# Kernel tuning notes

Hardware: AMD Instinct MI355X
Metric: run time of the kernel (lower is better)

The kernel has to match this reference:

```python
import jax, jax.numpy as jnp
import numpy as np

BS, NE, F = 128, 512, 6
HEADS, DPH = 4, 4
N_EMBD = HEADS * DPH  # 16


def setup_inputs() -> dict:
    key = jax.random.key(0)
    k_inp, k_mask, kq, kk, kv, kp = jax.random.split(key, 6)
    inp = jax.random.normal(k_inp, (BS, NE, F), dtype=jnp.float32)
    # binary float mask; guarantee at least one unmasked entity per batch row
    mask = (jax.random.uniform(k_mask, (BS, NE)) < 0.8).astype(jnp.float32)
    mask = mask.at[:, 0].set(1.0)
    std = 1.0 / np.sqrt(N_EMBD)
    Wq = jax.random.normal(kq, (N_EMBD, F), dtype=jnp.float32) * std
    Wk = jax.random.normal(kk, (N_EMBD, F), dtype=jnp.float32) * std
    Wv = jax.random.normal(kv, (N_EMBD, F), dtype=jnp.float32) * std
    Wpost = jax.random.normal(kp, (F, N_EMBD), dtype=jnp.float32) * std
    return {"inp": inp, "mask": mask, "Wq": Wq, "Wk": Wk, "Wv": Wv, "Wpost": Wpost}


def reference(inp, mask, Wq, Wk, Wv, Wpost):
    bs, ne, f = inp.shape
    x_in = inp * mask[:, :, None]                       # mask input entities
    # projections (Linear with weight [out,in]): x @ W.T
    q = (x_in @ Wq.T).reshape(bs, ne, HEADS, DPH)
    k = (x_in @ Wk.T).reshape(bs, ne, HEADS, DPH)
    v = (x_in @ Wv.T).reshape(bs, ne, HEADS, DPH)
    scale = 1.0 / np.sqrt(N_EMBD / HEADS)               # 1/sqrt(4)
    logits = jnp.einsum('bqhd,bkhd->bhqk', q, k) * scale  # [bs,H,NE,NE]
    logits = logits + 1e9 * (mask[:, None, None, :] - 1.0)  # mask keys pre-softmax
    p = jax.nn.softmax(logits, axis=-1)
    p = p * mask[:, None, :, None]                      # zero masked query rows
    att = jnp.einsum('bhqk,bkhd->bqhd', p, v).reshape(bs, ne, N_EMBD)
    x = x_in + att @ Wpost.T                            # residual
    # mask-corrected mean/std normalization over dims [1,2]
    N = jnp.sum(mask, axis=1)[:, None, None]            # [bs,1,1] valid entity count
    mu = jnp.mean(x, axis=(1, 2), keepdims=True) * (ne / N)
    x2 = x + (1.0 - mask[:, :, None]) * mu              # fill masked slots with mu
    m2 = jnp.mean(x2, axis=(1, 2), keepdims=True)
    var = jnp.sum((x2 - m2) ** 2, axis=(1, 2), keepdims=True) / (ne * f - 1)  # unbiased
    std = jnp.sqrt(var) * jnp.sqrt((f * ne - 1.0) / (f * N - 1.0))
    xn = (x - mu) / (std + 1e-6)
    # masked mean pool over entities
    summed = jnp.sum(xn * mask[:, :, None], axis=1)     # [bs,F]
    denom = jnp.sum(mask, axis=1)[:, None]
    return summed / denom
```

## Files before the change

kernel.cpp:

```cpp
#include <hip/hip_runtime.h>
#include <math.h>

#define BS    128
#define NE    512
#define F     6
#define NH    4
#define DPH   4
#define NEMBD 16

#if __has_builtin(__builtin_amdgcn_exp2f)
#define EXP2(x) __builtin_amdgcn_exp2f(x)
#else
#define EXP2(x) exp2f(x)
#endif

typedef float v2f __attribute__((ext_vector_type(2)));

#define CH    8
#define CKEYS 64
#define CPAD  65

__global__ __launch_bounds__(256) void attn_kernel(
    const float* __restrict__ inp, const float* __restrict__ mask,
    const float* __restrict__ Wq, const float* __restrict__ Wk,
    const float* __restrict__ Wv, float* __restrict__ att_out)
{
    const int blk  = blockIdx.x;
    const int b    = blk >> 3;
    const int h    = (blk >> 1) & 3;
    const int half = blk & 1;
    const int t    = threadIdx.x;
    const int c    = t & 7;
    const int g    = t >> 3;

    __shared__ float4 sk[CH * CPAD];
    __shared__ float4 sv[CH * CPAD];
    __shared__ float  sn[4];

    float mw = 0.f;
    #pragma unroll
    for (int s = 0; s < 2; ++s) {
        const int e = t + s * 256;
        const float me = mask[b * NE + e];
        mw += me;
        const float2* rp = (const float2*)(inp + ((size_t)(b * NE + e)) * F);
        const float2 r0 = rp[0], r1 = rp[1], r2 = rp[2];
        const float x0 = r0.x * me, x1 = r0.y * me, x2 = r1.x * me,
                    x3 = r1.y * me, x4 = r2.x * me, x5 = r2.y * me;
        const float* wk = Wk + h * DPH * F;
        const float* wv = Wv + h * DPH * F;
        float kk[DPH], vv[DPH];
        #pragma unroll
        for (int d = 0; d < DPH; ++d) {
            const float* w = wk + d * F;
            kk[d] = x0*w[0] + x1*w[1] + x2*w[2] + x3*w[3] + x4*w[4] + x5*w[5];
            w = wv + d * F;
            vv[d] = x0*w[0] + x1*w[1] + x2*w[2] + x3*w[3] + x4*w[4] + x5*w[5];
        }
        sk[(e >> 6) * CPAD + (e & 63)] = make_float4(kk[0], kk[1], kk[2], kk[3]);
        sv[(e >> 6) * CPAD + (e & 63)] = make_float4(vv[0], vv[1], vv[2], vv[3]);
    }
    #pragma unroll
    for (int off = 32; off >= 1; off >>= 1) mw += __shfl_down(mw, off);
    if ((t & 63) == 0) sn[t >> 6] = mw;

    const float QS = 0.5f * 1.44269504088896340736f;
    v2f qv[4][DPH];
    {
        const float* wq = Wq + h * DPH * F;
        #pragma unroll
        for (int r = 0; r < 8; ++r) {
            const int row = half * 256 + 8 * g + r;
            const float mr = mask[b * NE + row];
            const float2* rp = (const float2*)(inp + ((size_t)(b * NE + row)) * F);
            const float2 r0 = rp[0], r1 = rp[1], r2 = rp[2];
            const float x0 = r0.x * mr, x1 = r0.y * mr, x2 = r1.x * mr,
                        x3 = r1.y * mr, x4 = r2.x * mr, x5 = r2.y * mr;
            #pragma unroll
            for (int d = 0; d < DPH; ++d) {
                const float* w = wq + d * F;
                const float qd = QS * (x0*w[0] + x1*w[1] + x2*w[2] + x3*w[3] + x4*w[4] + x5*w[5]);
                if (r & 1) qv[r >> 1][d].y = qd; else qv[r >> 1][d].x = qd;
            }
        }
    }

    __syncthreads();

    const float Nb = sn[0] + sn[1] + sn[2] + sn[3];
    const float lcorr = 512.0f - Nb;

    const float4* kb = sk + c * CPAD;
    const float4* vb = sv + c * CPAD;
    v2f l2[4], a2[4][DPH];
    #pragma unroll
    for (int p = 0; p < 4; ++p) {
        l2[p] = (v2f)(0.f);
        #pragma unroll
        for (int d = 0; d < DPH; ++d) a2[p][d] = (v2f)(0.f);
    }

    #pragma unroll 4
    for (int j = 0; j < CKEYS; ++j) {
        const float4 kv = kb[j];
        const float4 uv = vb[j];
        const v2f kx = (v2f){kv.x, kv.x}, ky = (v2f){kv.y, kv.y},
                  kz = (v2f){kv.z, kv.z}, kw = (v2f){kv.w, kv.w};
        const v2f ux = (v2f){uv.x, uv.x}, uy = (v2f){uv.y, uv.y},
                  uz = (v2f){uv.z, uv.z}, uw = (v2f){uv.w, uv.w};
        #pragma unroll
        for (int p = 0; p < 4; ++p) {
            v2f s = qv[p][3] * kw;
            s = __builtin_elementwise_fma(qv[p][2], kz, s);
            s = __builtin_elementwise_fma(qv[p][1], ky, s);
            s = __builtin_elementwise_fma(qv[p][0], kx, s);
            v2f e;
            e.x = EXP2(s.x);
            e.y = EXP2(s.y);
            l2[p] += e;
            a2[p][0] = __builtin_elementwise_fma(e, ux, a2[p][0]);
            a2[p][1] = __builtin_elementwise_fma(e, uy, a2[p][1]);
            a2[p][2] = __builtin_elementwise_fma(e, uz, a2[p][2]);
            a2[p][3] = __builtin_elementwise_fma(e, uw, a2[p][3]);
        }
    }

    #pragma unroll
    for (int m = 1; m <= 4; m <<= 1) {
        #pragma unroll
        for (int p = 0; p < 4; ++p) {
            l2[p].x += __shfl_xor(l2[p].x, m);
            l2[p].y += __shfl_xor(l2[p].y, m);
            #pragma unroll
            for (int d = 0; d < DPH; ++d) {
                a2[p][d].x += __shfl_xor(a2[p][d].x, m);
                a2[p][d].y += __shfl_xor(a2[p][d].y, m);
            }
        }
    }

    float lsel = l2[0].x, p0 = a2[0][0].x, p1 = a2[0][1].x,
          p2 = a2[0][2].x, p3 = a2[0][3].x;
    #pragma unroll
    for (int r = 1; r < 8; ++r) {
        if (r == c) {
            const int pp = r >> 1;
            if (r & 1) {
                lsel = l2[pp].y; p0 = a2[pp][0].y; p1 = a2[pp][1].y;
                p2 = a2[pp][2].y; p3 = a2[pp][3].y;
            } else {
                lsel = l2[pp].x; p0 = a2[pp][0].x; p1 = a2[pp][1].x;
                p2 = a2[pp][2].x; p3 = a2[pp][3].x;
            }
        }
    }

    const int row = half * 256 + 8 * g + c;
    const float mi = mask[b * NE + row];
    const float rs = mi / (lsel - lcorr);
    float4* o = (float4*)(att_out + ((size_t)(b * NE + row)) * NEMBD + h * DPH);
    *o = make_float4(p0 * rs, p1 * rs, p2 * rs, p3 * rs);
}

__global__ __launch_bounds__(NE) void epi_kernel(
    const float* __restrict__ inp, const float* __restrict__ mask,
    const float* __restrict__ Wpost, const float* __restrict__ att,
    float* __restrict__ out)
{
    const int b = blockIdx.x;
    const int i = threadIdx.x;
    const int wave = i >> 6;
    const int lane = i & 63;

    __shared__ float swp[F * NEMBD];
    __shared__ float red[64];

    if (i < F * NEMBD) swp[i] = Wpost[i];
    __syncthreads();

    const float mi = mask[b * NE + i];
    const float* row = inp + ((size_t)(b * NE + i)) * F;
    const float* ar  = att + ((size_t)(b * NE + i)) * NEMBD;

    float a[NEMBD];
    #pragma unroll
    for (int t = 0; t < NEMBD; t += 4) {
        const float4 v = *(const float4*)(ar + t);
        a[t] = v.x; a[t+1] = v.y; a[t+2] = v.z; a[t+3] = v.w;
    }

    float x[F];
    #pragma unroll
    for (int f = 0; f < F; ++f) {
        float acc = row[f] * mi;
        #pragma unroll
        for (int t = 0; t < NEMBD; ++t) acc = fmaf(a[t], swp[f * NEMBD + t], acc);
        x[f] = acc;
    }

    float rsum = x[0] + x[1] + x[2] + x[3] + x[4] + x[5];
    float rn = mi;
    #pragma unroll
    for (int off = 32; off >= 1; off >>= 1) {
        rsum += __shfl_down(rsum, off);
        rn   += __shfl_down(rn, off);
    }
    if (lane == 0) { red[wave * 2] = rsum; red[wave * 2 + 1] = rn; }
    __syncthreads();
    float S = 0.f, N = 0.f;
    #pragma unroll
    for (int w = 0; w < 8; ++w) { S += red[w * 2]; N += red[w * 2 + 1]; }

    const float mu     = S / (6.0f * N);
    const float sum_x2 = S + (NE - N) * 6.0f * mu;
    const float m2     = sum_x2 / (NE * 6.0f);
    const float add    = (1.0f - mi) * mu;

    float ss = 0.f;
    #pragma unroll
    for (int f = 0; f < F; ++f) { const float d = x[f] + add - m2; ss = fmaf(d, d, ss); }

    __syncthreads();
    #pragma unroll
    for (int off = 32; off >= 1; off >>= 1) ss += __shfl_down(ss, off);
    if (lane == 0) red[wave] = ss;
    __syncthreads();
    float vs = 0.f;
    #pragma unroll
    for (int w = 0; w < 8; ++w) vs += red[w];

    const float var  = vs / (NE * 6.0f - 1.0f);
    const float stdv = sqrtf(var) * sqrtf((6.0f * NE - 1.0f) / (6.0f * N - 1.0f));
    const float inv  = 1.0f / (stdv + 1e-6f);

    float y[F];
    #pragma unroll
    for (int f = 0; f < F; ++f) y[f] = mi * (x[f] - mu) * inv;

    __syncthreads();
    #pragma unroll
    for (int off = 32; off >= 1; off >>= 1) {
        #pragma unroll
        for (int f = 0; f < F; ++f) y[f] += __shfl_down(y[f], off);
    }
    if (lane == 0) {
        #pragma unroll
        for (int f = 0; f < F; ++f) red[wave * F + f] = y[f];
    }
    __syncthreads();
    if (i < F) {
        float tt = 0.f;
        #pragma unroll
        for (int w = 0; w < 8; ++w) tt += red[w * F + i];
        out[b * F + i] = tt / N;
    }
}

extern "C" void kernel_launch(void* const* d_in, const int* in_sizes, int n_in,
                              void* d_out, int out_size, void* d_ws, size_t ws_size,
                              hipStream_t stream) {
    const float* inp   = (const float*)d_in[0];
    const float* mask  = (const float*)d_in[1];
    const float* Wq    = (const float*)d_in[2];
    const float* Wk    = (const float*)d_in[3];
    const float* Wv    = (const float*)d_in[4];
    const float* Wpost = (const float*)d_in[5];
    float* out = (float*)d_out;
    float* att = (float*)d_ws;

    attn_kernel<<<BS * NH * 2, 256, 0, stream>>>(inp, mask, Wq, Wk, Wv, att);
    epi_kernel <<<BS, NE, 0, stream>>>(inp, mask, Wpost, att, out);
}
```

Baseline: 103.8 us.

## Compact unmasked entities so attention only iterates over active keys and queries

The attention kernel now uses a ballot and an atomic prefix to compact the unmasked entities into contiguous shared-memory slots. Q, K and V are computed only for active entities, and each thread loops over L = ceil(Nk/8) keys instead of all 64, with a correction for zero-padded slots. Waves whose query slots are all beyond Nk exit early. Blocks are merged from 2x256 to one 512-thread block per (batch, head) so each block sees every entity. Masked rows are no longer written, so the epilogue multiplies the attention input by the mask to ignore stale workspace values. In exchange this adds an atomic, extra barriers and shared-memory zeroing, and reduces the number of blocks.

```diff
diff --git a/kernel.cpp b/kernel.cpp
--- a/kernel.cpp
+++ b/kernel.cpp
@@ -8,6 +8,9 @@
 #define DPH   4
 #define NEMBD 16
 
+#define CH    8
+#define CPAD  65
+
 #if __has_builtin(__builtin_amdgcn_exp2f)
 #define EXP2(x) __builtin_amdgcn_exp2f(x)
 #else
@@ -16,79 +19,91 @@
 
 typedef float v2f __attribute__((ext_vector_type(2)));
 
-#define CH    8
-#define CKEYS 64
-#define CPAD  65
-
-__global__ __launch_bounds__(256) void attn_kernel(
+__global__ __launch_bounds__(512) void attn_kernel(
     const float* __restrict__ inp, const float* __restrict__ mask,
     const float* __restrict__ Wq, const float* __restrict__ Wk,
     const float* __restrict__ Wv, float* __restrict__ att_out)
 {
-    const int blk  = blockIdx.x;
-    const int b    = blk >> 3;
-    const int h    = (blk >> 1) & 3;
-    const int half = blk & 1;
+    const int b    = blockIdx.x >> 2;
+    const int h    = blockIdx.x & 3;
     const int t    = threadIdx.x;
     const int c    = t & 7;
     const int g    = t >> 3;
+    const int w    = t >> 6;
+    const int lane = t & 63;
 
     __shared__ float4 sk[CH * CPAD];
     __shared__ float4 sv[CH * CPAD];
-    __shared__ float  sn[4];
-
-    float mw = 0.f;
-    #pragma unroll
-    for (int s = 0; s < 2; ++s) {
-        const int e = t + s * 256;
-        const float me = mask[b * NE + e];
-        mw += me;
-        const float2* rp = (const float2*)(inp + ((size_t)(b * NE + e)) * F);
+    __shared__ float4 sq[576];
+    __shared__ unsigned short rlist[512];
+    __shared__ int scnt;
+    __shared__ int swb[8];
+
+    const float4 z4 = make_float4(0.f, 0.f, 0.f, 0.f);
+    sk[c * CPAD + g] = z4;
+    sv[c * CPAD + g] = z4;
+    sq[9 * g + c]    = z4;
+    if (t == 0) scnt = 0;
+
+    const float me = mask[b * NE + t];
+    const bool act = me > 0.f;
+
+    __syncthreads();
+
+    const unsigned long long ball = __ballot(act);
+    const unsigned int blo = (unsigned int)ball;
+    const unsigned int bhi = (unsigned int)(ball >> 32);
+    const int prefix = __builtin_amdgcn_mbcnt_hi(bhi,
+                        __builtin_amdgcn_mbcnt_lo(blo, 0));
+    if (lane == 0) swb[w] = atomicAdd(&scnt, (int)__popcll(ball));
+
+    __syncthreads();
+
+    const int Nk = scnt;
+    const int L  = (Nk + 7) >> 3;
+    const float lcorr = (float)(8 * L - Nk);
+
+    if (act) {
+        const int s = swb[w] + prefix;
+        const float2* rp = (const float2*)(inp + ((size_t)(b * NE + t)) * F);
         const float2 r0 = rp[0], r1 = rp[1], r2 = rp[2];
-        const float x0 = r0.x * me, x1 = r0.y * me, x2 = r1.x * me,
-                    x3 = r1.y * me, x4 = r2.x * me, x5 = r2.y * me;
+        const float x0 = r0.x, x1 = r0.y, x2 = r1.x,
+                    x3 = r1.y, x4 = r2.x, x5 = r2.y;
         const float* wk = Wk + h * DPH * F;
         const float* wv = Wv + h * DPH * F;
-        float kk[DPH], vv[DPH];
+        const float* wq = Wq + h * DPH * F;
+        const float QS = 0.5f * 1.44269504088896340736f;
+        float kk[4], vv[4], qq[4];
         #pragma unroll
         for (int d = 0; d < DPH; ++d) {
-            const float* w = wk + d * F;
-            kk[d] = x0*w[0] + x1*w[1] + x2*w[2] + x3*w[3] + x4*w[4] + x5*w[5];
-            w = wv + d * F;
-            vv[d] = x0*w[0] + x1*w[1] + x2*w[2] + x3*w[3] + x4*w[4] + x5*w[5];
-        }
-        sk[(e >> 6) * CPAD + (e & 63)] = make_float4(kk[0], kk[1], kk[2], kk[3]);
-        sv[(e >> 6) * CPAD + (e & 63)] = make_float4(vv[0], vv[1], vv[2], vv[3]);
-    }
-    #pragma unroll
-    for (int off = 32; off >= 1; off >>= 1) mw += __shfl_down(mw, off);
-    if ((t & 63) == 0) sn[t >> 6] = mw;
-
-    const float QS = 0.5f * 1.44269504088896340736f;
+            const float* wd = wk + d * F;
+            kk[d] = x0*wd[0] + x1*wd[1] + x2*wd[2] + x3*wd[3] + x4*wd[4] + x5*wd[5];
+            wd = wv + d * F;
+            vv[d] = x0*wd[0] + x1*wd[1] + x2*wd[2] + x3*wd[3] + x4*wd[4] + x5*wd[5];
+            wd = wq + d * F;
+            qq[d] = QS * (x0*wd[0] + x1*wd[1] + x2*wd[2] + x3*wd[3] + x4*wd[4] + x5*wd[5]);
+        }
+        sk[(s & 7) * CPAD + (s >> 3)] = make_float4(kk[0], kk[1], kk[2], kk[3]);
+        sv[(s & 7) * CPAD + (s >> 3)] = make_float4(vv[0], vv[1], vv[2], vv[3]);
+        sq[9 * (s >> 3) + (s & 7)]    = make_float4(qq[0], qq[1], qq[2], qq[3]);
+        rlist[s] = (unsigned short)t;
+    }
+
+    __syncthreads();
+
+    if (64 * w >= Nk) return;
+
+    float4 qa[8];
+    #pragma unroll
+    for (int r = 0; r < 8; ++r) qa[r] = sq[9 * g + r];
     v2f qv[4][DPH];
-    {
-        const float* wq = Wq + h * DPH * F;
-        #pragma unroll
-        for (int r = 0; r < 8; ++r) {
-            const int row = half * 256 + 8 * g + r;
-            const float mr = mask[b * NE + row];
-            const float2* rp = (const float2*)(inp + ((size_t)(b * NE + row)) * F);
-            const float2 r0 = rp[0], r1 = rp[1], r2 = rp[2];
-            const float x0 = r0.x * mr, x1 = r0.y * mr, x2 = r1.x * mr,
-                        x3 = r1.y * mr, x4 = r2.x * mr, x5 = r2.y * mr;
-            #pragma unroll
-            for (int d = 0; d < DPH; ++d) {
-                const float* w = wq + d * F;
-                const float qd = QS * (x0*w[0] + x1*w[1] + x2*w[2] + x3*w[3] + x4*w[4] + x5*w[5]);
-                if (r & 1) qv[r >> 1][d].y = qd; else qv[r >> 1][d].x = qd;
-            }
-        }
-    }
-
-    __syncthreads();
-
-    const float Nb = sn[0] + sn[1] + sn[2] + sn[3];
-    const float lcorr = 512.0f - Nb;
+    #pragma unroll
+    for (int p = 0; p < 4; ++p) {
+        qv[p][0] = (v2f){qa[2*p].x, qa[2*p+1].x};
+        qv[p][1] = (v2f){qa[2*p].y, qa[2*p+1].y};
+        qv[p][2] = (v2f){qa[2*p].z, qa[2*p+1].z};
+        qv[p][3] = (v2f){qa[2*p].w, qa[2*p+1].w};
+    }
 
     const float4* kb = sk + c * CPAD;
     const float4* vb = sv + c * CPAD;
@@ -101,7 +116,7 @@
     }
 
     #pragma unroll 4
-    for (int j = 0; j < CKEYS; ++j) {
+    for (int j = 0; j < L; ++j) {
         const float4 kv = kb[j];
         const float4 uv = vb[j];
         const v2f kx = (v2f){kv.x, kv.x}, ky = (v2f){kv.y, kv.y},
@@ -155,11 +170,13 @@
         }
     }
 
-    const int row = half * 256 + 8 * g + c;
-    const float mi = mask[b * NE + row];
-    const float rs = mi / (lsel - lcorr);
-    float4* o = (float4*)(att_out + ((size_t)(b * NE + row)) * NEMBD + h * DPH);
-    *o = make_float4(p0 * rs, p1 * rs, p2 * rs, p3 * rs);
+    const int slot = 8 * g + c;
+    if (slot < Nk) {
+        const int row = rlist[slot];
+        const float rs = 1.0f / (lsel - lcorr);
+        float4* o = (float4*)(att_out + ((size_t)(b * NE + row)) * NEMBD + h * DPH);
+        *o = make_float4(p0 * rs, p1 * rs, p2 * rs, p3 * rs);
+    }
 }
 
 __global__ __launch_bounds__(NE) void epi_kernel(
@@ -186,7 +203,7 @@
     #pragma unroll
     for (int t = 0; t < NEMBD; t += 4) {
         const float4 v = *(const float4*)(ar + t);
-        a[t] = v.x; a[t+1] = v.y; a[t+2] = v.z; a[t+3] = v.w;
+        a[t] = v.x * mi; a[t+1] = v.y * mi; a[t+2] = v.z * mi; a[t+3] = v.w * mi;
     }
 
     float x[F];
@@ -268,6 +285,6 @@
     float* out = (float*)d_out;
     float* att = (float*)d_ws;
 
-    attn_kernel<<<BS * NH * 2, 256, 0, stream>>>(inp, mask, Wq, Wk, Wv, att);
+    attn_kernel<<<BS * NH, 512, 0, stream>>>(inp, mask, Wq, Wk, Wv, att);
     epi_kernel <<<BS, NE, 0, stream>>>(inp, mask, Wpost, att, out);
 }
```

Result: faster. 95.45 us (-8.0%).
